# Performance work log

Hardware: AMD Instinct MI355X
Metric: run time of the kernel (lower is better)

Reference implementation:

```python
import jax, jax.numpy as jnp
import numpy as np

B_IN, C_OUT, K, P, STRIDE, ITERS = 32, 32, 3, 4, 2, 3
PSIZE = P * P
EPS = 1e-08
LAMBDA = 0.001
LN_2PI = float(np.log(2.0 * np.pi))


def _patch(t, K, stride):
    # t: (b, h, w, B, d) -> (b, oh, ow, K, K, B, d)
    b, h, w, B, d = t.shape
    oh = (h - K + 1) // stride
    idxs = jnp.arange(oh)[:, None] * stride + jnp.arange(K)[None, :]  # (oh, K)
    t = t[:, idxs]            # (b, oh, K, w, B, d)
    t = t[:, :, :, idxs]      # (b, oh, K, ow, K, B, d)
    t = jnp.transpose(t, (0, 1, 3, 2, 4, 5, 6))  # (b, oh, ow, K, K, B, d)
    return t, oh, oh


def _em_routing(v, a_in, beta_u, beta_a):
    # v: (b,h,w,Bn,C,psize); a_in: (b,h,w,Bn,1)
    b, h, w, Bn, C, psize = v.shape
    mu = sigma_sq = a_out = None
    for it in range(ITERS):
        if it == 0:
            r = jnp.full((b, h, w, Bn, C), 1.0 / C, dtype=v.dtype) * a_in
        else:
            ln_pjh = -((v - mu) ** 2) / (2.0 * sigma_sq) - 0.5 * jnp.log(sigma_sq) - 0.5 * LN_2PI
            ln_ap = ln_pjh.sum(axis=5) + jnp.log(a_out.reshape(b, h, w, 1, C))
            r = jax.nn.softmax(ln_ap, axis=4)
        r_sum = r.sum(axis=3, keepdims=True)                 # (b,h,w,1,C)
        coeff = (r / (r_sum + EPS))[..., None]               # (b,h,w,Bn,C,1)
        mu = jnp.sum(coeff * v, axis=3, keepdims=True)       # (b,h,w,1,C,psize)
        sigma_sq = jnp.sum(coeff * (v - mu) ** 2, axis=3, keepdims=True)
        r_sum6 = r_sum[..., None]                            # (b,h,w,1,C,1)
        cost_h = (beta_u + 0.5 * jnp.log(sigma_sq)) * r_sum6 # log(sqrt(s)) = 0.5*log(s)
        a_out = jax.nn.sigmoid(LAMBDA * (beta_a - cost_h.sum(axis=5, keepdims=True)))
    return mu.reshape(b, h, w, C, psize), a_out.reshape(b, h, w, C, 1)


def setup_inputs() -> dict:
    key = jax.random.key(0)
    k1, k2, k3 = jax.random.split(key, 3)
    b, h, w = 16, 14, 14
    x = jax.random.normal(k1, (b, h, w, B_IN, PSIZE), dtype=jnp.float32)
    a = jax.random.uniform(k2, (b, h, w, B_IN, 1), dtype=jnp.float32)
    weights = jax.random.normal(k3, (1, 1, 1, K * K * B_IN, C_OUT, P, P), dtype=jnp.float32)
    beta_u = jnp.zeros((C_OUT, 1), dtype=jnp.float32)
    beta_a = jnp.zeros((C_OUT, 1), dtype=jnp.float32)
    return {"x": x, "a": a, "weights": weights, "beta_u": beta_u, "beta_a": beta_a}


def reference(x, a, weights, beta_u, beta_a):
    b = x.shape[0]
    p_in, oh, ow = _patch(x, K, STRIDE)
    a_in, _, _ = _patch(a, K, STRIDE)
    KKB = K * K * B_IN
    p_in = p_in.reshape(b, oh, ow, KKB, PSIZE)
    a_in = a_in.reshape(b, oh, ow, KKB, 1)
    # voting: per-capsule PxP pose matmul with transformation matrices
    pose = p_in.reshape(b, oh, ow, KKB, P, P)
    W = weights.reshape(KKB, C_OUT, P, P)
    v = jnp.einsum('bhwnij,ncjl->bhwncil', pose, W).reshape(b, oh, ow, KKB, C_OUT, PSIZE)
    return _em_routing(v, a_in, beta_u, beta_a)
```

## Files before the change

### kernel.cpp

```cpp
#include <hip/hip_runtime.h>


#define LN2PI 1.8378770664093453f
#define LOG2E 1.4426950408889634f

typedef __attribute__((ext_vector_type(2))) float f32x2;
#define FMA2(a, b, c) __builtin_elementwise_fma((a), (b), (c))
__device__ __forceinline__ f32x2 splat2(float x) { f32x2 r; r.x = x; r.y = x; return r; }

#define DPP_ADD(x, ctrl) \
    ((x) + __int_as_float(__builtin_amdgcn_update_dpp( \
        0, __float_as_int(x), (ctrl), 0xF, 0xF, true)))

__device__ __forceinline__ float sum32(float e) {
    float s = e;
    s = DPP_ADD(s, 0xB1);
    s = DPP_ADD(s, 0x4E);
    s = DPP_ADD(s, 0x141);
    s = DPP_ADD(s, 0x140);
    s += __shfl_xor(s, 16);
    return s;
}

__global__ __launch_bounds__(256)
void wtrans(const float4* __restrict__ W4, float4* __restrict__ Wt)
{
    int idx = blockIdx.x * 256 + threadIdx.x;
    if (idx < 36864) {
        int n = idx >> 7;
        int r = idx & 127;
        int c = r >> 2, q = r & 3;
        Wt[((n * 4 + q) << 5) + c] = W4[idx];
    }
}

__global__ __launch_bounds__(256)
void em_fused(const float* __restrict__ x,
              const float* __restrict__ a,
              const float4* __restrict__ Wt,
              const float* __restrict__ bu,
              const float* __restrict__ ba,
              float* __restrict__ out)
{
    __shared__ float ain_s[288];
    __shared__ float SA[2][32][17];
    __shared__ float SB[2][32][17];
    __shared__ f32x2 php_s[32][9];
    __shared__ f32x2 mh_s[32][9];
    __shared__ float A_s[32];
    __shared__ float AU_s[32];

    const int tid  = threadIdx.x;
    const int wv   = tid >> 6;
    const int lane = tid & 63;
    const int half = (lane >> 5) & 1;
    const int c    = lane & 31;

    const int pos = blockIdx.x;
    const int b   = pos / 36;
    const int rem = pos % 36;
    const int oy  = rem / 6, ox = rem % 6;
    const int iy0 = oy * 2, ix0 = ox * 2;

    const float4* x4 = (const float4*)x;

    for (int idx = tid; idx < 288; idx += 256) {
        int seg = idx >> 5, bi = idx & 31;
        int kh = seg / 3, kw = seg % 3;
        ain_s[idx] = a[((b * 14 + iy0 + kh) * 14 + (ix0 + kw)) * 32 + bi] * 0.03125f;
    }
    __syncthreads();

    const int n0 = wv * 72 + half;

    for (int it = 0; it < 3; ++it) {
        f32x2 ph[8], mh[8];
        float Ac = 0.f;
        if (it > 0) {
            #pragma unroll
            for (int j = 0; j < 8; ++j) { ph[j] = php_s[c][j]; mh[j] = mh_s[c][j]; }
            float AU = AU_s[c];
            float m = AU;
            #pragma unroll
            for (int mk = 16; mk >= 1; mk >>= 1)
                m = fmaxf(m, __shfl_xor(m, mk));
            Ac = A_s[c] - m;
        }

        f32x2 s1[8], s2[8];
        #pragma unroll
        for (int j = 0; j < 8; ++j) { s1[j] = splat2(0.f); s2[j] = splat2(0.f); }
        float Racc = 0.f;

        const float4* wp = Wt + (size_t)n0 * 128 + c;
        const float* an  = ain_s + n0;

        int n = n0;
        const float4* px;
        {
            int seg = n >> 5, bi = n & 31;
            int kh = (seg * 86) >> 8;
            int kw = seg - 3 * kh;
            px = x4 + ((size_t)((b * 14 + iy0 + kh) * 14 + (ix0 + kw)) * 32 + bi) * 4;
        }

        for (int s = 0; s < 36; ++s) {
            float4 wr0 = wp[0], wr1 = wp[32], wr2 = wp[64], wr3 = wp[96];
            float4 pr0 = px[0], pr1 = px[1], pr2 = px[2], pr3 = px[3];

            f32x2 w2[8];
            w2[0].x = wr0.x; w2[0].y = wr0.y;  w2[1].x = wr0.z; w2[1].y = wr0.w;
            w2[2].x = wr1.x; w2[2].y = wr1.y;  w2[3].x = wr1.z; w2[3].y = wr1.w;
            w2[4].x = wr2.x; w2[4].y = wr2.y;  w2[5].x = wr2.z; w2[5].y = wr2.w;
            w2[6].x = wr3.x; w2[6].y = wr3.y;  w2[7].x = wr3.z; w2[7].y = wr3.w;

            f32x2 v2[8];
            #pragma unroll
            for (int i = 0; i < 4; ++i) {
                float4 pr = (i == 0) ? pr0 : (i == 1) ? pr1 : (i == 2) ? pr2 : pr3;
                #pragma unroll
                for (int lp = 0; lp < 2; ++lp) {
                    f32x2 t = splat2(pr.x) * w2[0 + lp];
                    t = FMA2(splat2(pr.y), w2[2 + lp], t);
                    t = FMA2(splat2(pr.z), w2[4 + lp], t);
                    t = FMA2(splat2(pr.w), w2[6 + lp], t);
                    v2[i * 2 + lp] = t;
                }
            }

            float r;
            if (it == 0) {
                r = an[2 * s];
            } else {
                f32x2 acc2 = splat2(0.f);
                acc2.x = Ac;
                #pragma unroll
                for (int j = 0; j < 8; ++j) {
                    f32x2 t = FMA2(ph[j], v2[j], mh[j]);
                    acc2 = FMA2(t, v2[j], acc2);
                }
                float e = __builtin_amdgcn_exp2f(acc2.x + acc2.y);
                float ssum = sum32(e);
                r = __fdividef(e, ssum + 1e-30f);
            }

            Racc += r;
            f32x2 rr = splat2(r);
            #pragma unroll
            for (int j = 0; j < 8; ++j) {
                f32x2 rv = rr * v2[j];
                s1[j] = s1[j] + rv;
                s2[j] = FMA2(rv, v2[j], s2[j]);
            }

            wp += 256;
            n += 2;
            if ((n & 31) < 2) {
                int seg = n >> 5, bi = n & 31;
                int kh = (seg * 86) >> 8;
                int kw = seg - 3 * kh;
                px = x4 + ((size_t)((b * 14 + iy0 + kh) * 14 + (ix0 + kw)) * 32 + bi) * 4;
            } else {
                px += 8;
            }
        }

        #pragma unroll
        for (int j = 0; j < 8; ++j) {
            s1[j].x += __shfl_xor(s1[j].x, 32);
            s1[j].y += __shfl_xor(s1[j].y, 32);
            s2[j].x += __shfl_xor(s2[j].x, 32);
            s2[j].y += __shfl_xor(s2[j].y, 32);
        }
        Racc += __shfl_xor(Racc, 32);

        if (wv >= 2) {
            const int row = wv - 2;
            if (half == 0) {
                #pragma unroll
                for (int j = 0; j < 8; ++j) {
                    SA[row][c][2 * j]     = s1[j].x;
                    SA[row][c][2 * j + 1] = s1[j].y;
                }
                SA[row][c][16] = Racc;
            } else {
                #pragma unroll
                for (int j = 0; j < 8; ++j) {
                    SB[row][c][2 * j]     = s2[j].x;
                    SB[row][c][2 * j + 1] = s2[j].y;
                }
            }
        }
        __syncthreads();
        if (wv < 2) {
            if (half == 0) {
                #pragma unroll
                for (int j = 0; j < 8; ++j) {
                    SA[wv][c][2 * j]     += s1[j].x;
                    SA[wv][c][2 * j + 1] += s1[j].y;
                }
                SA[wv][c][16] += Racc;
            } else {
                #pragma unroll
                for (int j = 0; j < 8; ++j) {
                    SB[wv][c][2 * j]     += s2[j].x;
                    SB[wv][c][2 * j + 1] += s2[j].y;
                }
            }
        }
        __syncthreads();

        {
            const int cf = tid >> 3, k2 = tid & 7;
            float R = SA[0][cf][16] + SA[1][cf][16];
            float rinv = __fdividef(1.f, R + 1e-8f);
            float muv[2];
            float tpart = 0.f, Ks = 0.f;
            #pragma unroll
            for (int t2 = 0; t2 < 2; ++t2) {
                int k = k2 + t2 * 8;
                float sv1 = SA[0][cf][k] + SA[1][cf][k];
                float sv2 = SB[0][cf][k] + SB[1][cf][k];
                float mu  = sv1 * rinv;
                float sig = fmaf(-mu, mu, sv2 * rinv);
                sig = fmaxf(sig, 1e-30f);
                float p = __fdividef(0.5f, sig);
                muv[t2] = mu;
                if (it < 2) {
                    ((float*)&php_s[cf][0])[k] = -p * LOG2E;
                    ((float*)&mh_s[cf][0])[k]  = 2.f * p * mu * LOG2E;
                }
                tpart += __logf(sig);
                Ks = fmaf(p * mu, mu, Ks);
            }
            #pragma unroll
            for (int mk = 4; mk >= 1; mk >>= 1) {
                tpart += __shfl_xor(tpart, mk);
                Ks    += __shfl_xor(Ks, mk);
            }
            float cost = R * fmaf(0.5f, tpart, 16.f * bu[cf]);
            float aout = __fdividef(1.f, 1.f + __expf(-(0.001f * (ba[cf] - cost))));

            if (it < 2) {
                if (k2 == 0) {
                    float Afold = __logf(aout) - 0.5f * tpart - 8.0f * LN2PI - Ks;
                    A_s[cf]  = Afold * LOG2E;
                    AU_s[cf] = (Afold + Ks) * LOG2E;
                }
            } else {
                out[(size_t)pos * 512 + cf * 16 + k2]     = muv[0];
                out[(size_t)pos * 512 + cf * 16 + k2 + 8] = muv[1];
                if (k2 == 0)
                    out[294912 + pos * 32 + cf] = aout;
            }
        }
        __syncthreads();
    }
}

#define NB 288
#define LNSTEP 36
__global__ __launch_bounds__(256, 2)
void convcaps_em_legacy(const float* __restrict__ x, const float* __restrict__ a,
                        const float* __restrict__ W, const float* __restrict__ bu,
                        const float* __restrict__ ba, float* __restrict__ out)
{
    __shared__ __align__(16) float pose_s[NB * 16];
    __shared__ __align__(16) float ain_s[NB];
    __shared__ float S1w[4][32][17];
    __shared__ float S2w[4][32][17];
    __shared__ float Rw[4][32];
    __shared__ float mu_s[32][17];
    __shared__ float p_s[32][17];
    __shared__ float A_s[32];

    const int tid = threadIdx.x, wv = tid >> 6, lane = tid & 63;
    const int half = (lane >> 5) & 1, c = lane & 31;
    const int bid = blockIdx.x, b = bid / 36, rem = bid % 36;
    const int oy = rem / 6, ox = rem % 6, iy0 = oy * 2, ix0 = ox * 2;
    {
        const float4* x4 = (const float4*)x;
        float4* d4 = (float4*)pose_s;
        for (int idx = tid; idx < 1152; idx += 256) {
            int seg = idx >> 7, u = idx & 127, kh = seg / 3, kw = seg % 3;
            d4[idx] = x4[((b * 14 + iy0 + kh) * 14 + (ix0 + kw)) * 128 + u];
        }
        const float4* a4 = (const float4*)a;
        float4* e4 = (float4*)ain_s;
        if (tid < 72) {
            int seg = tid >> 3, u = tid & 7, kh = seg / 3, kw = seg % 3;
            e4[tid] = a4[((b * 14 + iy0 + kh) * 14 + (ix0 + kw)) * 8 + u];
        }
    }
    __syncthreads();
    const float4* W4 = (const float4*)W;
    float muh[16], ph[16], Ac = 0.0f;
    #pragma unroll
    for (int i = 0; i < 16; ++i) { muh[i] = 0.0f; ph[i] = 0.0f; }
    for (int iter = 0; iter < 3; ++iter) {
        if (iter > 0) {
            #pragma unroll
            for (int il = 0; il < 16; ++il) { muh[il] = mu_s[c][il]; ph[il] = p_s[c][il]; }
            Ac = A_s[c];
        }
        float S1[16], S2[16], Racc = 0.0f;
        #pragma unroll
        for (int i = 0; i < 16; ++i) { S1[i] = 0.0f; S2[i] = 0.0f; }
        for (int s = 0; s < LNSTEP; ++s) {
            const int n = wv * 72 + 2 * s + half;
            float wreg[16], preg[16];
            const float4* wp = W4 + (size_t)(n * 32 + c) * 4;
            float4 w0 = wp[0], w1 = wp[1], w2 = wp[2], w3 = wp[3];
            wreg[0]=w0.x; wreg[1]=w0.y; wreg[2]=w0.z; wreg[3]=w0.w;
            wreg[4]=w1.x; wreg[5]=w1.y; wreg[6]=w1.z; wreg[7]=w1.w;
            wreg[8]=w2.x; wreg[9]=w2.y; wreg[10]=w2.z; wreg[11]=w2.w;
            wreg[12]=w3.x; wreg[13]=w3.y; wreg[14]=w3.z; wreg[15]=w3.w;
            const float4* pp = (const float4*)&pose_s[n * 16];
            float4 p0 = pp[0], p1 = pp[1], p2 = pp[2], p3 = pp[3];
            preg[0]=p0.x; preg[1]=p0.y; preg[2]=p0.z; preg[3]=p0.w;
            preg[4]=p1.x; preg[5]=p1.y; preg[6]=p1.z; preg[7]=p1.w;
            preg[8]=p2.x; preg[9]=p2.y; preg[10]=p2.z; preg[11]=p2.w;
            preg[12]=p3.x; preg[13]=p3.y; preg[14]=p3.z; preg[15]=p3.w;
            float v[16];
            #pragma unroll
            for (int i = 0; i < 4; ++i)
                #pragma unroll
                for (int l = 0; l < 4; ++l) {
                    float acc = preg[i*4+0] * wreg[l];
                    acc = fmaf(preg[i*4+1], wreg[4+l], acc);
                    acc = fmaf(preg[i*4+2], wreg[8+l], acc);
                    acc = fmaf(preg[i*4+3], wreg[12+l], acc);
                    v[i*4+l] = acc;
                }
            float r;
            if (iter == 0) r = ain_s[n] * 0.03125f;
            else {
                float acc = 0.0f;
                #pragma unroll
                for (int il = 0; il < 16; ++il) { float d = v[il]-muh[il]; acc = fmaf(-ph[il], d*d, acc); }
                float lnap = Ac + acc, m = lnap;
                #pragma unroll
                for (int mk = 16; mk >= 1; mk >>= 1) m = fmaxf(m, __shfl_xor(m, mk));
                float e = __expf(lnap - m), ssum = e;
                #pragma unroll
                for (int mk = 16; mk >= 1; mk >>= 1) ssum += __shfl_xor(ssum, mk);
                r = __fdividef(e, ssum);
            }
            Racc += r;
            #pragma unroll
            for (int il = 0; il < 16; ++il) { float rv = r * v[il]; S1[il] += rv; S2[il] = fmaf(rv, v[il], S2[il]); }
        }
        #pragma unroll
        for (int il = 0; il < 16; ++il) { S1[il] += __shfl_xor(S1[il], 32); S2[il] += __shfl_xor(S2[il], 32); }
        Racc += __shfl_xor(Racc, 32);
        if (half == 0) {
            #pragma unroll
            for (int il = 0; il < 16; ++il) { S1w[wv][c][il] = S1[il]; S2w[wv][c][il] = S2[il]; }
            Rw[wv][c] = Racc;
        }
        __syncthreads();
        {
            const int c2 = tid >> 3, k = tid & 7;
            float R = Rw[0][c2] + Rw[1][c2] + Rw[2][c2] + Rw[3][c2];
            float rinv = __fdividef(1.0f, R + 1e-8f);
            float muv[2], pv[2], tpart = 0.0f;
            #pragma unroll
            for (int t2 = 0; t2 < 2; ++t2) {
                int il = k + t2 * 8;
                float s1 = S1w[0][c2][il]+S1w[1][c2][il]+S1w[2][c2][il]+S1w[3][c2][il];
                float s2 = S2w[0][c2][il]+S2w[1][c2][il]+S2w[2][c2][il]+S2w[3][c2][il];
                float mu = s1 * rinv;
                float sig = fmaf(-mu, mu, s2 * rinv);
                sig = fmaxf(sig, 1e-30f);
                muv[t2] = mu; pv[t2] = __fdividef(0.5f, sig); tpart += __logf(sig);
            }
            #pragma unroll
            for (int mk = 4; mk >= 1; mk >>= 1) tpart += __shfl_xor(tpart, mk);
            float cost = R * fmaf(0.5f, tpart, 16.0f * bu[c2]);
            float aout = __fdividef(1.0f, 1.0f + __expf(-(0.001f * (ba[c2] - cost))));
            if (iter < 2) {
                #pragma unroll
                for (int t2 = 0; t2 < 2; ++t2) { int il = k + t2*8; mu_s[c2][il] = muv[t2]; p_s[c2][il] = pv[t2]; }
                if (k == 0) A_s[c2] = __logf(aout) - 0.5f * tpart - 8.0f * LN2PI;
            } else {
                #pragma unroll
                for (int t2 = 0; t2 < 2; ++t2) { int il = k + t2*8; out[(size_t)bid*512 + c2*16 + il] = muv[t2]; }
                if (k == 0) out[294912 + bid * 32 + c2] = aout;
            }
        }
        __syncthreads();
    }
}

extern "C" void kernel_launch(void* const* d_in, const int* in_sizes, int n_in,
                              void* d_out, int out_size, void* d_ws, size_t ws_size,
                              hipStream_t stream) {
    (void)in_sizes; (void)n_in; (void)out_size;
    const float* x  = (const float*)d_in[0];
    const float* a  = (const float*)d_in[1];
    const float* w  = (const float*)d_in[2];
    const float* bu = (const float*)d_in[3];
    const float* ba = (const float*)d_in[4];
    float* out = (float*)d_out;
    float* wsf = (float*)d_ws;

    if (ws_size >= (size_t)147456 * 4) {
        float* Wt = wsf;
        hipLaunchKernelGGL(wtrans, dim3(144), dim3(256), 0, stream,
                           (const float4*)w, (float4*)Wt);
        hipLaunchKernelGGL(em_fused, dim3(576), dim3(256), 0, stream,
                           x, a, (const float4*)Wt, bu, ba, out);
    } else {
        hipLaunchKernelGGL(convcaps_em_legacy, dim3(576), dim3(256), 0, stream,
                           x, a, w, bu, ba, out);
    }
}
```

Before: 96.83 us.

## Store weights as fp16 and stage pose patches in shared memory

The weight pre-transform kernel now converts the transformation matrices to half precision, which halves the per-iteration global weight traffic inside the fused routing kernel. Each block also loads its 3x3 patch of input poses into LDS once, so the inner loop no longer re-reads them from global memory. This removes the segment-boundary pointer logic. The cost is reduced weight precision, with the risk of accuracy deviation, plus about 18KB more shared memory per block, which could reduce occupancy.

New measurement: 89.70 us. 1.08x faster.

```diff
diff --git a/kernel.cpp b/kernel.cpp
--- a/kernel.cpp
+++ b/kernel.cpp
@@ -1,4 +1,5 @@
 #include <hip/hip_runtime.h>
+#include <hip/hip_fp16.h>
 
 
 #define LN2PI 1.8378770664093453f
@@ -22,26 +23,44 @@
     return s;
 }
 
+__device__ __forceinline__ f32x2 cvt2(unsigned int u) {
+    __half2 h = *reinterpret_cast<const __half2*>(&u);
+    f32x2 r; r.x = __low2float(h); r.y = __high2float(h);
+    return r;
+}
+
 __global__ __launch_bounds__(256)
-void wtrans(const float4* __restrict__ W4, float4* __restrict__ Wt)
+void wtrans16(const float4* __restrict__ W4, uint4* __restrict__ Wt16)
 {
     int idx = blockIdx.x * 256 + threadIdx.x;
-    if (idx < 36864) {
-        int n = idx >> 7;
-        int r = idx & 127;
-        int c = r >> 2, q = r & 3;
-        Wt[((n * 4 + q) << 5) + c] = W4[idx];
+    if (idx < 9216) {
+        int n = idx >> 5, c = idx & 31;
+        const float4* src = W4 + (size_t)(n * 32 + c) * 4;
+        float4 w0 = src[0], w1 = src[1], w2 = src[2], w3 = src[3];
+        uint4 o0, o1;
+        __half2 h;
+        h = __floats2half2_rn(w0.x, w0.y); o0.x = *reinterpret_cast<unsigned int*>(&h);
+        h = __floats2half2_rn(w0.z, w0.w); o0.y = *reinterpret_cast<unsigned int*>(&h);
+        h = __floats2half2_rn(w1.x, w1.y); o0.z = *reinterpret_cast<unsigned int*>(&h);
+        h = __floats2half2_rn(w1.z, w1.w); o0.w = *reinterpret_cast<unsigned int*>(&h);
+        h = __floats2half2_rn(w2.x, w2.y); o1.x = *reinterpret_cast<unsigned int*>(&h);
+        h = __floats2half2_rn(w2.z, w2.w); o1.y = *reinterpret_cast<unsigned int*>(&h);
+        h = __floats2half2_rn(w3.x, w3.y); o1.z = *reinterpret_cast<unsigned int*>(&h);
+        h = __floats2half2_rn(w3.z, w3.w); o1.w = *reinterpret_cast<unsigned int*>(&h);
+        Wt16[(size_t)(n * 2 + 0) * 32 + c] = o0;
+        Wt16[(size_t)(n * 2 + 1) * 32 + c] = o1;
     }
 }
 
 __global__ __launch_bounds__(256)
 void em_fused(const float* __restrict__ x,
               const float* __restrict__ a,
-              const float4* __restrict__ Wt,
+              const uint4* __restrict__ Wt16,
               const float* __restrict__ bu,
               const float* __restrict__ ba,
               float* __restrict__ out)
 {
+    __shared__ __align__(16) float4 pose_s[288 * 4];
     __shared__ float ain_s[288];
     __shared__ float SA[2][32][17];
     __shared__ float SB[2][32][17];
@@ -62,12 +81,18 @@
     const int oy  = rem / 6, ox = rem % 6;
     const int iy0 = oy * 2, ix0 = ox * 2;
 
-    const float4* x4 = (const float4*)x;
-
-    for (int idx = tid; idx < 288; idx += 256) {
-        int seg = idx >> 5, bi = idx & 31;
-        int kh = seg / 3, kw = seg % 3;
-        ain_s[idx] = a[((b * 14 + iy0 + kh) * 14 + (ix0 + kw)) * 32 + bi] * 0.03125f;
+    {
+        const float4* x4 = (const float4*)x;
+        for (int idx = tid; idx < 1152; idx += 256) {
+            int seg = idx >> 7, u = idx & 127;
+            int kh = seg / 3, kw = seg % 3;
+            pose_s[idx] = x4[((b * 14 + iy0 + kh) * 14 + (ix0 + kw)) * 128 + u];
+        }
+        for (int idx = tid; idx < 288; idx += 256) {
+            int seg = idx >> 5, bi = idx & 31;
+            int kh = seg / 3, kw = seg % 3;
+            ain_s[idx] = a[((b * 14 + iy0 + kh) * 14 + (ix0 + kw)) * 32 + bi] * 0.03125f;
+        }
     }
     __syncthreads();
 
@@ -92,27 +117,19 @@
         for (int j = 0; j < 8; ++j) { s1[j] = splat2(0.f); s2[j] = splat2(0.f); }
         float Racc = 0.f;
 
-        const float4* wp = Wt + (size_t)n0 * 128 + c;
+        const uint4* wp = Wt16 + (size_t)n0 * 64 + c;
+        const float4* pp = pose_s + n0 * 4;
         const float* an  = ain_s + n0;
 
-        int n = n0;
-        const float4* px;
-        {
-            int seg = n >> 5, bi = n & 31;
-            int kh = (seg * 86) >> 8;
-            int kw = seg - 3 * kh;
-            px = x4 + ((size_t)((b * 14 + iy0 + kh) * 14 + (ix0 + kw)) * 32 + bi) * 4;
-        }
-
         for (int s = 0; s < 36; ++s) {
-            float4 wr0 = wp[0], wr1 = wp[32], wr2 = wp[64], wr3 = wp[96];
-            float4 pr0 = px[0], pr1 = px[1], pr2 = px[2], pr3 = px[3];
+            uint4 ua = wp[0], ub = wp[32];
+            float4 pr0 = pp[0], pr1 = pp[1], pr2 = pp[2], pr3 = pp[3];
 
             f32x2 w2[8];
-            w2[0].x = wr0.x; w2[0].y = wr0.y;  w2[1].x = wr0.z; w2[1].y = wr0.w;
-            w2[2].x = wr1.x; w2[2].y = wr1.y;  w2[3].x = wr1.z; w2[3].y = wr1.w;
-            w2[4].x = wr2.x; w2[4].y = wr2.y;  w2[5].x = wr2.z; w2[5].y = wr2.w;
-            w2[6].x = wr3.x; w2[6].y = wr3.y;  w2[7].x = wr3.z; w2[7].y = wr3.w;
+            w2[0] = cvt2(ua.x); w2[1] = cvt2(ua.y);
+            w2[2] = cvt2(ua.z); w2[3] = cvt2(ua.w);
+            w2[4] = cvt2(ub.x); w2[5] = cvt2(ub.y);
+            w2[6] = cvt2(ub.z); w2[7] = cvt2(ub.w);
 
             f32x2 v2[8];
             #pragma unroll
@@ -153,16 +170,8 @@
                 s2[j] = FMA2(rv, v2[j], s2[j]);
             }
 
-            wp += 256;
-            n += 2;
-            if ((n & 31) < 2) {
-                int seg = n >> 5, bi = n & 31;
-                int kh = (seg * 86) >> 8;
-                int kw = seg - 3 * kh;
-                px = x4 + ((size_t)((b * 14 + iy0 + kh) * 14 + (ix0 + kw)) * 32 + bi) * 4;
-            } else {
-                px += 8;
-            }
+            wp += 128;
+            pp += 8;
         }
 
         #pragma unroll
@@ -402,14 +411,13 @@
     const float* bu = (const float*)d_in[3];
     const float* ba = (const float*)d_in[4];
     float* out = (float*)d_out;
-    float* wsf = (float*)d_ws;
-
-    if (ws_size >= (size_t)147456 * 4) {
-        float* Wt = wsf;
-        hipLaunchKernelGGL(wtrans, dim3(144), dim3(256), 0, stream,
-                           (const float4*)w, (float4*)Wt);
+
+    if (ws_size >= (size_t)294912) {
+        uint4* Wt16 = (uint4*)d_ws;
+        hipLaunchKernelGGL(wtrans16, dim3(36), dim3(256), 0, stream,
+                           (const float4*)w, Wt16);
         hipLaunchKernelGGL(em_fused, dim3(576), dim3(256), 0, stream,
-                           x, a, (const float4*)Wt, bu, ba, out);
+                           x, a, (const uint4*)Wt16, bu, ba, out);
     } else {
         hipLaunchKernelGGL(convcaps_em_legacy, dim3(576), dim3(256), 0, stream,
                            x, a, w, bu, ba, out);
```
